# Kernel optimization log

Hardware: AMD Instinct MI355X
Metric: run time of the kernel (lower is better)

Reference implementation:

```python
import jax, jax.numpy as jnp
import numpy as np

NUM_HEADS = 12
DIM = 768


def setup_inputs() -> dict:
    key = jax.random.key(0)
    ks = jax.random.split(key, 7)
    B, S, E = 8, 1024, DIM
    s = 0.02
    return {
        "x": jax.random.normal(ks[0], (B, S, E), dtype=jnp.float32),
        "Wq": jax.random.normal(ks[1], (E, E), dtype=jnp.float32) * s,
        "bq": jnp.zeros((E,), dtype=jnp.float32),
        "Wk": jax.random.normal(ks[2], (E, E), dtype=jnp.float32) * s,
        "bk": jnp.zeros((E,), dtype=jnp.float32),
        "Wo": jax.random.normal(ks[3], (E, E), dtype=jnp.float32) * s,
        "bo": jnp.zeros((E,), dtype=jnp.float32),
    }


def reference(x, Wq, bq, Wk, bk, Wo, bo):
    B, S, E = x.shape
    n = NUM_HEADS
    d = E // n
    scale = d ** (-0.5)

    def heads(t):  # [B,S,E] -> [B,n,S,d]
        return t.reshape(B, S, n, d).transpose(0, 2, 1, 3)

    q = heads(x @ Wq.T + bq)
    k = heads(x @ Wk.T + bk)
    v = k  # faithful to source bug: v = self.k_w(x)

    attn = jnp.einsum('bnqd,bnkd->bnqk', q, k) * scale  # [B,n,S,S]
    attn = jax.nn.softmax(attn, axis=-1)
    out = jnp.einsum('bnqk,bnkd->bnqd', attn, v)  # [B,n,S,d]
    out = out.transpose(0, 2, 1, 3).reshape(B, S, E)
    return out @ Wo.T + bo
```

## Files before the change

kernel.cpp:

```cpp
#include <hip/hip_runtime.h>
#include <stdint.h>


using short8   = __attribute__((ext_vector_type(8))) short;
using uint4v   = __attribute__((ext_vector_type(4))) unsigned;
using float4v  = __attribute__((ext_vector_type(4))) float;
using float16v = __attribute__((ext_vector_type(16))) float;

struct __align__(8) U2 { unsigned x, y; };

__device__ __forceinline__ void async16(void* lds, const void* g) {
  __builtin_amdgcn_global_load_lds(
      (const __attribute__((address_space(1))) void*)g,
      (__attribute__((address_space(3))) void*)lds, 16, 0, 0);
}

__device__ __forceinline__ unsigned bf16b(float f) {
  union { float f; unsigned u; } v; v.f = f;
  unsigned r = v.u + 0x7FFFu + ((v.u >> 16) & 1u);
  return r >> 16;
}
__device__ __forceinline__ unsigned rne_adj(float f) {
  union { float f; unsigned u; } v; v.f = f;
  return v.u + 0x7FFFu + ((v.u >> 16) & 1u);
}
__device__ __forceinline__ unsigned pack_hi16(unsigned a, unsigned b) {
  return __builtin_amdgcn_perm(a, b, 0x07060302u);
}

__global__ __launch_bounds__(256) void cvt_bf16(const float* __restrict__ in,
                                                unsigned short* __restrict__ out,
                                                int n8) {
  int i = blockIdx.x * 256 + threadIdx.x;
  if (i >= n8) return;
  const float4v* p = (const float4v*)in;
  float4v a = p[i * 2], b = p[i * 2 + 1];
  uint4v w;
  w[0] = pack_hi16(rne_adj(a[1]), rne_adj(a[0]));
  w[1] = pack_hi16(rne_adj(a[3]), rne_adj(a[2]));
  w[2] = pack_hi16(rne_adj(b[1]), rne_adj(b[0]));
  w[3] = pack_hi16(rne_adj(b[3]), rne_adj(b[2]));
  ((uint4v*)out)[i] = w;
}

__global__ __launch_bounds__(256) void cvt_w3(const float* __restrict__ w0,
                                              const float* __restrict__ w1,
                                              const float* __restrict__ w2,
                                              unsigned short* __restrict__ o0,
                                              unsigned short* __restrict__ o1,
                                              unsigned short* __restrict__ o2) {
  int mi = blockIdx.x / 288;
  int i = (blockIdx.x - mi * 288) * 256 + threadIdx.x;
  const float* in = (mi == 0) ? w0 : (mi == 1) ? w1 : w2;
  unsigned short* out = (mi == 0) ? o0 : (mi == 1) ? o1 : o2;
  const float4v* p = (const float4v*)in;
  float4v a = p[i * 2], b = p[i * 2 + 1];
  uint4v w;
  w[0] = pack_hi16(rne_adj(a[1]), rne_adj(a[0]));
  w[1] = pack_hi16(rne_adj(a[3]), rne_adj(a[2]));
  w[2] = pack_hi16(rne_adj(b[1]), rne_adj(b[0]));
  w[3] = pack_hi16(rne_adj(b[3]), rne_adj(b[2]));
  ((uint4v*)out)[i] = w;
}

__global__ __launch_bounds__(256, 3) void sgemm_qk(
    const unsigned short* __restrict__ A, const unsigned short* __restrict__ B,
    const float* __restrict__ bias0, const float* __restrict__ bias1,
    unsigned short* __restrict__ outq, unsigned short* __restrict__ outk,
    unsigned short* __restrict__ outkt) {
  __shared__ __align__(16) unsigned short a_l[8192];
  __shared__ __align__(16) unsigned short b_l[8192];
  const int tid = threadIdx.x;
  const int w = tid >> 6, lane = tid & 63;
  const int Q4 = lane >> 4, r = lane & 15;
  const int m0 = blockIdx.y * 128;
  const int n0 = blockIdx.x * 128;
  const int wm = w >> 1, wn = w & 1;

  float4v acc[4][4];
#pragma unroll
  for (int i = 0; i < 4; ++i)
#pragma unroll
    for (int j = 0; j < 4; ++j)
#pragma unroll
      for (int g = 0; g < 4; ++g) acc[i][j][g] = 0.0f;

  const unsigned short* Ab = A + (size_t)(m0 + r) * 768 + Q4 * 8;
  const unsigned short* Bb = B + (size_t)(n0 + r) * 768 + Q4 * 8;

  for (int kt = 0; kt < 768; kt += 64) {
    __syncthreads();
#pragma unroll
    for (int ci = 0; ci < 4; ++ci) {
      int idx = w * 4 + ci;
      int c = idx >> 1, kh = idx & 1;
      async16(&a_l[idx * 512 + lane * 8], Ab + c * 16 * 768 + kt + kh * 32);
      async16(&b_l[idx * 512 + lane * 8], Bb + c * 16 * 768 + kt + kh * 32);
    }
    __syncthreads();

    short8 af[4][2], bf[4][2];
#pragma unroll
    for (int i = 0; i < 4; ++i)
#pragma unroll
      for (int ks = 0; ks < 2; ++ks) {
        af[i][ks] = *(const short8*)&a_l[((wm * 4 + i) * 2 + ks) * 512 + lane * 8];
        bf[i][ks] = *(const short8*)&b_l[((wn * 4 + i) * 2 + ks) * 512 + lane * 8];
      }
#pragma unroll
    for (int mt = 0; mt < 4; ++mt)
#pragma unroll
      for (int nt = 0; nt < 4; ++nt)
#pragma unroll
        for (int ks = 0; ks < 2; ++ks)
          acc[mt][nt] = __builtin_amdgcn_mfma_f32_16x16x32_bf16(
              af[mt][ks], bf[nt][ks], acc[mt][nt], 0, 0, 0);
  }

  const bool isq = (n0 < 768);
  const float* bias = isq ? bias0 : bias1;
  unsigned short* outp = isq ? outq : outk;
  const int nb = isq ? n0 : (n0 - 768);
  const float scl = isq ? 0.18033688011112042f : 1.0f;
#pragma unroll
  for (int nt = 0; nt < 4; ++nt) {
    int n = nb + wn * 64 + nt * 16 + r;
    float bv = bias[n];
#pragma unroll
    for (int mt = 0; mt < 4; ++mt) {
      int m = m0 + wm * 64 + mt * 16 + Q4 * 4;
#pragma unroll
      for (int g = 0; g < 4; ++g)
        outp[(size_t)(m + g) * 768 + n] = (unsigned short)bf16b((acc[mt][nt][g] + bv) * scl);
    }
  }
  if (!isq) {
    const int bq = m0 >> 10;
    const int sbase = (m0 & 1023) + wm * 64 + (Q4 & 1) * 8 + (Q4 >> 1) * 4;
#pragma unroll
    for (int nt = 0; nt < 4; ++nt) {
      int n = nb + wn * 64 + nt * 16 + r;
      int hh = n >> 6, dd = n & 63;
      float bv = bias[n];
#pragma unroll
      for (int mt = 0; mt < 4; ++mt) {
        int ns = sbase + mt * 16;
        unsigned lo = pack_hi16(rne_adj(acc[mt][nt][1] + bv), rne_adj(acc[mt][nt][0] + bv));
        unsigned hi = pack_hi16(rne_adj(acc[mt][nt][3] + bv), rne_adj(acc[mt][nt][2] + bv));
        *(U2*)(outkt + (size_t)((bq * 12 + hh) * 64 + dd) * 1024 + ns) = U2{lo, hi};
      }
    }
  }
}

__global__ __launch_bounds__(256, 3) void sgemm_out(
    const unsigned short* __restrict__ A, const unsigned short* __restrict__ B,
    const float* __restrict__ bias, float* __restrict__ outp) {
  __shared__ __align__(16) unsigned short a_l[4096];
  __shared__ __align__(16) unsigned short b_l[8192];
  const int tid = threadIdx.x;
  const int w = tid >> 6, lane = tid & 63;
  const int Q4 = lane >> 4, r = lane & 15;
  const int m0 = blockIdx.y * 64;
  const int n0 = blockIdx.x * 128;
  const int wm = w >> 1, wn = w & 1;

  float4v acc[2][4];
#pragma unroll
  for (int i = 0; i < 2; ++i)
#pragma unroll
    for (int j = 0; j < 4; ++j)
#pragma unroll
      for (int g = 0; g < 4; ++g) acc[i][j][g] = 0.0f;

  const unsigned short* Ab = A + (size_t)(m0 + r) * 768 + Q4 * 8;
  const unsigned short* Bb = B + (size_t)(n0 + r) * 768 + Q4 * 8;

  for (int kt = 0; kt < 768; kt += 64) {
    __syncthreads();
#pragma unroll
    for (int ci = 0; ci < 2; ++ci) {
      int idx = w * 2 + ci;
      int c = idx >> 1, kh = idx & 1;
      async16(&a_l[idx * 512 + lane * 8], Ab + c * 16 * 768 + kt + kh * 32);
    }
#pragma unroll
    for (int ci = 0; ci < 4; ++ci) {
      int idx = w * 4 + ci;
      int c = idx >> 1, kh = idx & 1;
      async16(&b_l[idx * 512 + lane * 8], Bb + c * 16 * 768 + kt + kh * 32);
    }
    __syncthreads();

    short8 af[2][2], bf[4][2];
#pragma unroll
    for (int i = 0; i < 2; ++i)
#pragma unroll
      for (int ks = 0; ks < 2; ++ks)
        af[i][ks] = *(const short8*)&a_l[((wm * 2 + i) * 2 + ks) * 512 + lane * 8];
#pragma unroll
    for (int i = 0; i < 4; ++i)
#pragma unroll
      for (int ks = 0; ks < 2; ++ks)
        bf[i][ks] = *(const short8*)&b_l[((wn * 4 + i) * 2 + ks) * 512 + lane * 8];
#pragma unroll
    for (int mt = 0; mt < 2; ++mt)
#pragma unroll
      for (int nt = 0; nt < 4; ++nt)
#pragma unroll
        for (int ks = 0; ks < 2; ++ks)
          acc[mt][nt] = __builtin_amdgcn_mfma_f32_16x16x32_bf16(
              af[mt][ks], bf[nt][ks], acc[mt][nt], 0, 0, 0);
  }

#pragma unroll
  for (int nt = 0; nt < 4; ++nt) {
    int n = n0 + wn * 64 + nt * 16 + r;
    float bv = bias[n];
#pragma unroll
    for (int mt = 0; mt < 2; ++mt) {
      int m = m0 + wm * 32 + mt * 16 + Q4 * 4;
#pragma unroll
      for (int g = 0; g < 4; ++g)
        outp[(size_t)(m + g) * 768 + n] = acc[mt][nt][g] + bv;
    }
  }
}

__global__ __launch_bounds__(256, 3) void attn_fused(
    const unsigned short* __restrict__ qg,
    const unsigned short* __restrict__ kg,
    const unsigned short* __restrict__ ktg,
    unsigned short* __restrict__ ao) {
  __shared__ __align__(16) unsigned short q_l[8192];
  __shared__ __align__(16) unsigned short k_l[8192];
  __shared__ __align__(16) unsigned short vt_l[8192];

  const int tid = threadIdx.x;
  const int w = tid >> 6, lane = tid & 63;
  const int l31 = lane & 31, hi = lane >> 5;
  const int bid = blockIdx.x;
  const int b = bid & 7;
  const int h = bid >> 6;
  const int qt = (bid >> 3) & 7;
  const int q0 = qt * 128;
  const int bh = b * 12 + h;

#pragma unroll
  for (int ci = 0; ci < 4; ++ci) {
    int c = w * 4 + ci;
    async16(&q_l[c * 512 + lane * 8],
            qg + ((size_t)(b * 1024 + q0 + (c >> 2) * 32 + l31) * 768 + h * 64 + (c & 3) * 16 + hi * 8));
    async16(&k_l[c * 512 + lane * 8],
            kg + ((size_t)(b * 1024 + (c >> 2) * 32 + l31) * 768 + h * 64 + (c & 3) * 16 + hi * 8));
    async16(&vt_l[c * 512 + lane * 8],
            ktg + ((size_t)(bh * 64 + (c >> 3) * 32 + l31) * 1024 + (c & 7) * 16 + hi * 8));
  }
  __syncthreads();

  short8 bfq[4];
#pragma unroll
  for (int kb = 0; kb < 4; ++kb)
    bfq[kb] = *(const short8*)&q_l[(w * 4 + kb) * 512 + lane * 8];

  float16v o_acc[2];
#pragma unroll
  for (int db = 0; db < 2; ++db)
#pragma unroll
    for (int e = 0; e < 16; ++e) o_acc[db][e] = 0.0f;
  float ps = 0.0f;

#pragma unroll 1
  for (int it = 0; it < 8; ++it) {
    if (it > 0) {
      const int s0 = it * 128;
      __syncthreads();
#pragma unroll
      for (int ci = 0; ci < 4; ++ci) {
        int c = w * 4 + ci;
        async16(&k_l[c * 512 + lane * 8],
                kg + ((size_t)(b * 1024 + s0 + (c >> 2) * 32 + l31) * 768 + h * 64 + (c & 3) * 16 + hi * 8));
        async16(&vt_l[c * 512 + lane * 8],
                ktg + ((size_t)(bh * 64 + (c >> 3) * 32 + l31) * 1024 + s0 + (c & 7) * 16 + hi * 8));
      }
      __syncthreads();
    }

    float16v sc[4];
#pragma unroll
    for (int sb = 0; sb < 4; ++sb)
#pragma unroll
      for (int e = 0; e < 16; ++e) sc[sb][e] = 0.0f;
#pragma unroll
    for (int sb = 0; sb < 4; ++sb)
#pragma unroll
      for (int kb = 0; kb < 4; ++kb) {
        short8 af = *(const short8*)&k_l[(sb * 4 + kb) * 512 + lane * 8];
        sc[sb] = __builtin_amdgcn_mfma_f32_32x32x16_bf16(af, bfq[kb], sc[sb], 0, 0, 0);
      }

#pragma unroll
    for (int sb = 0; sb < 4; ++sb) {
      float pe[16];
#pragma unroll
      for (int e = 0; e < 16; ++e) pe[e] = __builtin_amdgcn_exp2f(sc[sb][e]);
#pragma unroll
      for (int e = 0; e < 16; ++e) ps += pe[e];
      uint4v w0, w1;
#pragma unroll
      for (int p = 0; p < 4; ++p) {
        w0[p] = pack_hi16(rne_adj(pe[2 * p + 1]), rne_adj(pe[2 * p]));
        w1[p] = pack_hi16(rne_adj(pe[2 * p + 9]), rne_adj(pe[2 * p + 8]));
      }
      short8 pf0 = __builtin_bit_cast(short8, w0);
      short8 pf1 = __builtin_bit_cast(short8, w1);
#pragma unroll
      for (int db = 0; db < 2; ++db) {
        short8 vf0 = *(const short8*)&vt_l[(db * 8 + sb * 2) * 512 + lane * 8];
        o_acc[db] = __builtin_amdgcn_mfma_f32_32x32x16_bf16(vf0, pf0, o_acc[db], 0, 0, 0);
        short8 vf1 = *(const short8*)&vt_l[(db * 8 + sb * 2 + 1) * 512 + lane * 8];
        o_acc[db] = __builtin_amdgcn_mfma_f32_32x32x16_bf16(vf1, pf1, o_acc[db], 0, 0, 0);
      }
    }
  }

  ps += __shfl_xor(ps, 32, 64);
  const float inv = 1.0f / ps;
  const size_t rowbase = (size_t)(b * 1024 + q0 + w * 32 + l31) * 768 + h * 64;
#pragma unroll
  for (int db = 0; db < 2; ++db)
#pragma unroll
    for (int qq = 0; qq < 4; ++qq) {
      unsigned lo = pack_hi16(rne_adj(o_acc[db][qq * 4 + 1] * inv),
                              rne_adj(o_acc[db][qq * 4 + 0] * inv));
      unsigned hh = pack_hi16(rne_adj(o_acc[db][qq * 4 + 3] * inv),
                              rne_adj(o_acc[db][qq * 4 + 2] * inv));
      *(U2*)(ao + rowbase + db * 32 + qq * 8 + hi * 4) = U2{lo, hh};
    }
}

extern "C" void kernel_launch(void* const* d_in, const int* in_sizes, int n_in,
                              void* d_out, int out_size, void* d_ws, size_t ws_size,
                              hipStream_t stream) {
  const float* x  = (const float*)d_in[0];
  const float* Wq = (const float*)d_in[1];
  const float* bq = (const float*)d_in[2];
  const float* Wk = (const float*)d_in[3];
  const float* bk = (const float*)d_in[4];
  const float* Wo = (const float*)d_in[5];
  const float* bo = (const float*)d_in[6];
  (void)in_sizes; (void)n_in; (void)out_size; (void)ws_size;

  char* ws = (char*)d_ws;
  unsigned short* x_b   = (unsigned short*)(ws);
  unsigned short* wqk_b = (unsigned short*)(ws + 12582912);
  unsigned short* wo_b  = (unsigned short*)(ws + 14942208);
  unsigned short* q_b   = (unsigned short*)(ws + 16121856);
  unsigned short* k_b   = (unsigned short*)(ws + 28704768);
  unsigned short* kt_b  = (unsigned short*)(ws + 41287680);
  unsigned short* ao_b  = (unsigned short*)(ws + 53870592);

  cvt_bf16<<<3072, 256, 0, stream>>>(x, x_b, 786432);
  cvt_w3<<<864, 256, 0, stream>>>(Wq, Wk, Wo, wqk_b, wqk_b + 589824, wo_b);

  sgemm_qk<<<dim3(12, 64), 256, 0, stream>>>(x_b, wqk_b, bq, bk, q_b, k_b, kt_b);
  attn_fused<<<768, 256, 0, stream>>>(q_b, k_b, kt_b, ao_b);
  sgemm_out<<<dim3(6, 128), 256, 0, stream>>>(ao_b, wo_b, bo, (float*)d_out);
}
```

Baseline: 203.8 us.

## Double-buffer LDS in QK projection GEMM with async loads and manual waitcnt

Rewrites the sgemm_qk main loop to use two LDS buffers. Async global-to-LDS loads for the next K tiles are issued before the MFMA work on the current tile, with manual vmcnt/lgkmcnt waits and barriers replacing the two __syncthreads per iteration. Each wave now stages only the rows it consumes. The grid is also transposed so consecutive blocks walk along M sharing the same weight tile, and the occupancy hint drops from 3 to 2 blocks per CU because LDS use doubles. The hand-placed wait counts assume 16 outstanding loads per stage, and a wrong count would cause races.

```diff
diff --git a/kernel.cpp b/kernel.cpp
--- a/kernel.cpp
+++ b/kernel.cpp
@@ -14,6 +14,10 @@
       (const __attribute__((address_space(1))) void*)g,
       (__attribute__((address_space(3))) void*)lds, 16, 0, 0);
 }
+
+#define VM_WAIT(n) asm volatile("s_waitcnt vmcnt(" #n ")" ::: "memory")
+#define LGKM_WAIT  asm volatile("s_waitcnt lgkmcnt(0)" ::: "memory")
+#define BARRIER    asm volatile("s_barrier" ::: "memory")
 
 __device__ __forceinline__ unsigned bf16b(float f) {
   union { float f; unsigned u; } v; v.f = f;
@@ -63,18 +67,18 @@
   ((uint4v*)out)[i] = w;
 }
 
-__global__ __launch_bounds__(256, 3) void sgemm_qk(
+__global__ __launch_bounds__(256, 2) void sgemm_qk(
     const unsigned short* __restrict__ A, const unsigned short* __restrict__ B,
     const float* __restrict__ bias0, const float* __restrict__ bias1,
     unsigned short* __restrict__ outq, unsigned short* __restrict__ outk,
     unsigned short* __restrict__ outkt) {
-  __shared__ __align__(16) unsigned short a_l[8192];
-  __shared__ __align__(16) unsigned short b_l[8192];
+  __shared__ __align__(16) unsigned short aB[2][8192];
+  __shared__ __align__(16) unsigned short bB[2][8192];
   const int tid = threadIdx.x;
   const int w = tid >> 6, lane = tid & 63;
   const int Q4 = lane >> 4, r = lane & 15;
-  const int m0 = blockIdx.y * 128;
-  const int n0 = blockIdx.x * 128;
+  const int m0 = blockIdx.x * 128;
+  const int n0 = blockIdx.y * 128;
   const int wm = w >> 1, wn = w & 1;
 
   float4v acc[4][4];
@@ -85,28 +89,32 @@
 #pragma unroll
       for (int g = 0; g < 4; ++g) acc[i][j][g] = 0.0f;
 
-  const unsigned short* Ab = A + (size_t)(m0 + r) * 768 + Q4 * 8;
-  const unsigned short* Bb = B + (size_t)(n0 + r) * 768 + Q4 * 8;
-
-  for (int kt = 0; kt < 768; kt += 64) {
-    __syncthreads();
-#pragma unroll
-    for (int ci = 0; ci < 4; ++ci) {
-      int idx = w * 4 + ci;
-      int c = idx >> 1, kh = idx & 1;
-      async16(&a_l[idx * 512 + lane * 8], Ab + c * 16 * 768 + kt + kh * 32);
-      async16(&b_l[idx * 512 + lane * 8], Bb + c * 16 * 768 + kt + kh * 32);
-    }
-    __syncthreads();
-
-    short8 af[4][2], bf[4][2];
+  const unsigned short* Abase = A + (size_t)(m0 + wm * 64 + r) * 768 + Q4 * 8;
+  const unsigned short* Bbase = B + (size_t)(n0 + wn * 64 + r) * 768 + Q4 * 8;
+
+  auto stage = [&](int buf, int kt) {
+#pragma unroll
+    for (int j = 0; j < 8; ++j)
+      async16(&aB[buf][(wm * 8 + j) * 512 + lane * 8],
+              Abase + (j >> 1) * (16 * 768) + kt + (j & 1) * 32);
+#pragma unroll
+    for (int j = 0; j < 8; ++j)
+      async16(&bB[buf][(wn * 8 + j) * 512 + lane * 8],
+              Bbase + (j >> 1) * (16 * 768) + kt + (j & 1) * 32);
+  };
+
+  short8 af[4][2], bf[4][2];
+  auto loadf = [&](int buf) {
 #pragma unroll
     for (int i = 0; i < 4; ++i)
 #pragma unroll
       for (int ks = 0; ks < 2; ++ks) {
-        af[i][ks] = *(const short8*)&a_l[((wm * 4 + i) * 2 + ks) * 512 + lane * 8];
-        bf[i][ks] = *(const short8*)&b_l[((wn * 4 + i) * 2 + ks) * 512 + lane * 8];
-      }
+        af[i][ks] = *(const short8*)&aB[buf][(wm * 8 + i * 2 + ks) * 512 + lane * 8];
+        bf[i][ks] = *(const short8*)&bB[buf][(wn * 8 + i * 2 + ks) * 512 + lane * 8];
+      }
+  };
+
+  auto dot = [&]() {
 #pragma unroll
     for (int mt = 0; mt < 4; ++mt)
 #pragma unroll
@@ -115,7 +123,16 @@
         for (int ks = 0; ks < 2; ++ks)
           acc[mt][nt] = __builtin_amdgcn_mfma_f32_16x16x32_bf16(
               af[mt][ks], bf[nt][ks], acc[mt][nt], 0, 0, 0);
-  }
+  };
+
+  stage(0, 0); stage(1, 64);
+#pragma unroll 1
+  for (int j = 0; j < 5; ++j) {
+    VM_WAIT(16); loadf(0); LGKM_WAIT; BARRIER; stage(0, j * 128 + 128); dot();
+    VM_WAIT(16); loadf(1); LGKM_WAIT; BARRIER; stage(1, j * 128 + 192); dot();
+  }
+  VM_WAIT(16); loadf(0); dot();
+  VM_WAIT(0);  loadf(1); dot();
 
   const bool isq = (n0 < 768);
   const float* bias = isq ? bias0 : bias1;
@@ -363,7 +380,7 @@
   cvt_bf16<<<3072, 256, 0, stream>>>(x, x_b, 786432);
   cvt_w3<<<864, 256, 0, stream>>>(Wq, Wk, Wo, wqk_b, wqk_b + 589824, wo_b);
 
-  sgemm_qk<<<dim3(12, 64), 256, 0, stream>>>(x_b, wqk_b, bq, bk, q_b, k_b, kt_b);
+  sgemm_qk<<<dim3(64, 12), 256, 0, stream>>>(x_b, wqk_b, bq, bk, q_b, k_b, kt_b);
   attn_fused<<<768, 256, 0, stream>>>(q_b, k_b, kt_b, ao_b);
   sgemm_out<<<dim3(6, 128), 256, 0, stream>>>(ao_b, wo_b, bo, (float*)d_out);
 }
```

After: 232.5 us. 1.14x slower.

## Register-prefetch next K tile in projection GEMMs and swap QK grid order

Applied to the files above, without the earlier changes.

Both projection GEMMs drop the async global-to-LDS copies bracketed by two syncthreads. They now load the next K tile into registers while the current tile is consumed, write it to LDS, and sync with raw s_waitcnt/s_barrier. The aim is to hide global load latency behind MFMA work. The QK GEMM grid is also transposed so consecutive blocks walk along M with a fixed weight tile, which may improve L2 reuse of weights. This costs extra VGPRs for staging, which could reduce occupancy, and relies on the hand-placed barriers being correct.

```diff
diff --git a/kernel.cpp b/kernel.cpp
--- a/kernel.cpp
+++ b/kernel.cpp
@@ -14,6 +14,9 @@
       (const __attribute__((address_space(1))) void*)g,
       (__attribute__((address_space(3))) void*)lds, 16, 0, 0);
 }
+
+#define LGKM_WAIT  asm volatile("s_waitcnt lgkmcnt(0)" ::: "memory")
+#define BARRIER    asm volatile("s_barrier" ::: "memory")
 
 __device__ __forceinline__ unsigned bf16b(float f) {
   union { float f; unsigned u; } v; v.f = f;
@@ -73,8 +76,8 @@
   const int tid = threadIdx.x;
   const int w = tid >> 6, lane = tid & 63;
   const int Q4 = lane >> 4, r = lane & 15;
-  const int m0 = blockIdx.y * 128;
-  const int n0 = blockIdx.x * 128;
+  const int m0 = blockIdx.x * 128;
+  const int n0 = blockIdx.y * 128;
   const int wm = w >> 1, wn = w & 1;
 
   float4v acc[4][4];
@@ -88,18 +91,26 @@
   const unsigned short* Ab = A + (size_t)(m0 + r) * 768 + Q4 * 8;
   const unsigned short* Bb = B + (size_t)(n0 + r) * 768 + Q4 * 8;
 
-  for (int kt = 0; kt < 768; kt += 64) {
-    __syncthreads();
+  uint4v ra[4], rb[4];
+  auto gload = [&](int kt) {
+#pragma unroll
+    for (int ci = 0; ci < 4; ++ci) {
+      int idx = w * 4 + ci, c = idx >> 1, kh = idx & 1;
+      ra[ci] = *(const uint4v*)(Ab + c * 12288 + kt + kh * 32);
+      rb[ci] = *(const uint4v*)(Bb + c * 12288 + kt + kh * 32);
+    }
+  };
+  auto swrite = [&]() {
 #pragma unroll
     for (int ci = 0; ci < 4; ++ci) {
       int idx = w * 4 + ci;
-      int c = idx >> 1, kh = idx & 1;
-      async16(&a_l[idx * 512 + lane * 8], Ab + c * 16 * 768 + kt + kh * 32);
-      async16(&b_l[idx * 512 + lane * 8], Bb + c * 16 * 768 + kt + kh * 32);
-    }
-    __syncthreads();
-
-    short8 af[4][2], bf[4][2];
+      *(uint4v*)&a_l[idx * 512 + lane * 8] = ra[ci];
+      *(uint4v*)&b_l[idx * 512 + lane * 8] = rb[ci];
+    }
+  };
+
+  short8 af[4][2], bf[4][2];
+  auto loadf = [&]() {
 #pragma unroll
     for (int i = 0; i < 4; ++i)
 #pragma unroll
@@ -107,6 +118,8 @@
         af[i][ks] = *(const short8*)&a_l[((wm * 4 + i) * 2 + ks) * 512 + lane * 8];
         bf[i][ks] = *(const short8*)&b_l[((wn * 4 + i) * 2 + ks) * 512 + lane * 8];
       }
+  };
+  auto dot = [&]() {
 #pragma unroll
     for (int mt = 0; mt < 4; ++mt)
 #pragma unroll
@@ -115,6 +128,18 @@
         for (int ks = 0; ks < 2; ++ks)
           acc[mt][nt] = __builtin_amdgcn_mfma_f32_16x16x32_bf16(
               af[mt][ks], bf[nt][ks], acc[mt][nt], 0, 0, 0);
+  };
+
+  gload(0);
+#pragma unroll 1
+  for (int t = 0; t < 12; ++t) {
+    if (t > 0) BARRIER;
+    swrite();
+    if (t < 11) gload(t * 64 + 64);
+    LGKM_WAIT;
+    BARRIER;
+    loadf();
+    dot();
   }
 
   const bool isq = (n0 < 768);
@@ -176,23 +201,34 @@
   const unsigned short* Ab = A + (size_t)(m0 + r) * 768 + Q4 * 8;
   const unsigned short* Bb = B + (size_t)(n0 + r) * 768 + Q4 * 8;
 
-  for (int kt = 0; kt < 768; kt += 64) {
-    __syncthreads();
+  uint4v ra[2], rb[4];
+  auto gload = [&](int kt) {
 #pragma unroll
     for (int ci = 0; ci < 2; ++ci) {
       int idx = w * 2 + ci;
-      int c = idx >> 1, kh = idx & 1;
-      async16(&a_l[idx * 512 + lane * 8], Ab + c * 16 * 768 + kt + kh * 32);
+      ra[ci] = *(const uint4v*)(Ab + (idx >> 1) * 12288 + kt + (idx & 1) * 32);
     }
 #pragma unroll
     for (int ci = 0; ci < 4; ++ci) {
       int idx = w * 4 + ci;
-      int c = idx >> 1, kh = idx & 1;
-      async16(&b_l[idx * 512 + lane * 8], Bb + c * 16 * 768 + kt + kh * 32);
-    }
-    __syncthreads();
-
-    short8 af[2][2], bf[4][2];
+      rb[ci] = *(const uint4v*)(Bb + (idx >> 1) * 12288 + kt + (idx & 1) * 32);
+    }
+  };
+  auto swrite = [&]() {
+#pragma unroll
+    for (int ci = 0; ci < 2; ++ci) {
+      int idx = w * 2 + ci;
+      *(uint4v*)&a_l[idx * 512 + lane * 8] = ra[ci];
+    }
+#pragma unroll
+    for (int ci = 0; ci < 4; ++ci) {
+      int idx = w * 4 + ci;
+      *(uint4v*)&b_l[idx * 512 + lane * 8] = rb[ci];
+    }
+  };
+
+  short8 af[2][2], bf[4][2];
+  auto loadf = [&]() {
 #pragma unroll
     for (int i = 0; i < 2; ++i)
 #pragma unroll
@@ -203,6 +239,8 @@
 #pragma unroll
       for (int ks = 0; ks < 2; ++ks)
         bf[i][ks] = *(const short8*)&b_l[((wn * 4 + i) * 2 + ks) * 512 + lane * 8];
+  };
+  auto dot = [&]() {
 #pragma unroll
     for (int mt = 0; mt < 2; ++mt)
 #pragma unroll
@@ -211,6 +249,18 @@
         for (int ks = 0; ks < 2; ++ks)
           acc[mt][nt] = __builtin_amdgcn_mfma_f32_16x16x32_bf16(
               af[mt][ks], bf[nt][ks], acc[mt][nt], 0, 0, 0);
+  };
+
+  gload(0);
+#pragma unroll 1
+  for (int t = 0; t < 12; ++t) {
+    if (t > 0) BARRIER;
+    swrite();
+    if (t < 11) gload(t * 64 + 64);
+    LGKM_WAIT;
+    BARRIER;
+    loadf();
+    dot();
   }
 
 #pragma unroll
@@ -363,7 +413,7 @@
   cvt_bf16<<<3072, 256, 0, stream>>>(x, x_b, 786432);
   cvt_w3<<<864, 256, 0, stream>>>(Wq, Wk, Wo, wqk_b, wqk_b + 589824, wo_b);
 
-  sgemm_qk<<<dim3(12, 64), 256, 0, stream>>>(x_b, wqk_b, bq, bk, q_b, k_b, kt_b);
+  sgemm_qk<<<dim3(64, 12), 256, 0, stream>>>(x_b, wqk_b, bq, bk, q_b, k_b, kt_b);
   attn_fused<<<768, 256, 0, stream>>>(q_b, k_b, kt_b, ao_b);
   sgemm_out<<<dim3(6, 128), 256, 0, stream>>>(ao_b, wo_b, bo, (float*)d_out);
 }
```

New measurement: 200.3 us. Within noise of the previous version (-1.7%).
